# Optimization experiments

Hardware: AMD Instinct MI355X
Metric: run time of the kernel (lower is better)

The kernel has to match this reference:

```python
import jax, jax.numpy as jnp
import numpy as np
import math

L_MAX = 4
NUM_LM = (L_MAX + 1) ** 2  # 25
DEG_OF_LM = np.repeat(np.arange(L_MAX + 1), 2 * np.arange(L_MAX + 1) + 1)
SL = [slice(l * l, (l + 1) * (l + 1)) for l in range(L_MAX + 1)]
CUTOFF = 5.0

def _lf(n):
    return math.lgamma(n + 1)

def _cg_complex(l1, m1, l2, m2, l3, m3):
    if m1 + m2 != m3 or l3 < abs(l1 - l2) or l3 > l1 + l2:
        return 0.0
    pre = 0.5 * (_lf(l1 + l2 - l3) + _lf(l1 - l2 + l3) + _lf(-l1 + l2 + l3)
                 - _lf(l1 + l2 + l3 + 1)
                 + _lf(l1 + m1) + _lf(l1 - m1) + _lf(l2 + m2) + _lf(l2 - m2)
                 + _lf(l3 + m3) + _lf(l3 - m3))
    kmin = max(0, l2 - l3 - m1, l1 - l3 + m2)
    kmax = min(l1 + l2 - l3, l1 - m1, l2 + m2)
    s = 0.0
    for k in range(kmin, kmax + 1):
        ln = (_lf(k) + _lf(l1 + l2 - l3 - k) + _lf(l1 - m1 - k) + _lf(l2 + m2 - k)
              + _lf(l3 - l2 + m1 + k) + _lf(l3 - l1 - m2 + k))
        s += (-1) ** k * math.exp(pre - ln)
    return math.sqrt(2 * l3 + 1) * s

def _build_real_cg():
    # complex CG (Racah) -> real-spherical-harmonic coupling coefficients
    Cc = np.zeros((NUM_LM, NUM_LM, NUM_LM), dtype=np.complex128)
    U = np.zeros((NUM_LM, NUM_LM), dtype=np.complex128)
    for l in range(L_MAX + 1):
        off = l * l + l
        U[off, off] = 1.0
        for m in range(1, l + 1):
            U[off + m, off + m] = (-1) ** m / np.sqrt(2)
            U[off + m, off - m] = 1 / np.sqrt(2)
            U[off - m, off - m] = 1j / np.sqrt(2)
            U[off - m, off + m] = -1j * (-1) ** m / np.sqrt(2)
    for l1 in range(L_MAX + 1):
        for l2 in range(L_MAX + 1):
            for l3 in range(abs(l1 - l2), min(L_MAX, l1 + l2) + 1):
                for m1 in range(-l1, l1 + 1):
                    for m2 in range(-l2, l2 + 1):
                        m3 = m1 + m2
                        if abs(m3) <= l3:
                            Cc[l1*l1+l1+m1, l2*l2+l2+m2, l3*l3+l3+m3] = _cg_complex(l1, m1, l2, m2, l3, m3)
    T = np.einsum('ia,jb,kc,abc->ijk', U, U, U.conj(), Cc)
    C = T.real + T.imag  # exactly one part is nonzero per entry
    C[np.abs(C) < 1e-12] = 0.0
    return C.astype(np.float32)

CG = jnp.asarray(_build_real_cg())
PATHS = [(l1, l2, l3) for l1 in range(L_MAX + 1) for l2 in range(L_MAX + 1)
         for l3 in range(abs(l1 - l2), min(L_MAX, l1 + l2) + 1)]

def real_sph_harm(u):
    x, y, z = u[..., 0], u[..., 1], u[..., 2]
    x2, y2, z2 = x*x, y*y, z*z
    pi = np.pi
    Y = [
        jnp.full_like(x, 0.5*np.sqrt(1/pi)),
        np.sqrt(3/(4*pi))*y, np.sqrt(3/(4*pi))*z, np.sqrt(3/(4*pi))*x,
        0.5*np.sqrt(15/pi)*x*y, 0.5*np.sqrt(15/pi)*y*z,
        0.25*np.sqrt(5/pi)*(3*z2-1), 0.5*np.sqrt(15/pi)*x*z,
        0.25*np.sqrt(15/pi)*(x2-y2),
        0.25*np.sqrt(35/(2*pi))*y*(3*x2-y2), 0.5*np.sqrt(105/pi)*x*y*z,
        0.25*np.sqrt(21/(2*pi))*y*(5*z2-1), 0.25*np.sqrt(7/pi)*z*(5*z2-3),
        0.25*np.sqrt(21/(2*pi))*x*(5*z2-1), 0.25*np.sqrt(105/pi)*z*(x2-y2),
        0.25*np.sqrt(35/(2*pi))*x*(x2-3*y2),
        0.75*np.sqrt(35/pi)*x*y*(x2-y2), 0.75*np.sqrt(35/(2*pi))*y*z*(3*x2-y2),
        0.75*np.sqrt(5/pi)*x*y*(7*z2-1), 0.75*np.sqrt(5/(2*pi))*y*z*(7*z2-3),
        (3/16)*np.sqrt(1/pi)*(35*z2*z2-30*z2+3),
        0.75*np.sqrt(5/(2*pi))*x*z*(7*z2-3),
        (3/8)*np.sqrt(5/pi)*(x2-y2)*(7*z2-1),
        0.75*np.sqrt(35/(2*pi))*x*z*(x2-3*y2),
        (3/16)*np.sqrt(35/pi)*(x2*x2-6*x2*y2+y2*y2),
    ]
    return jnp.stack(Y, axis=-1)  # [..., 25]

def degree_dense(x, W):
    # equivariant per-(parity, degree) dense: x [N,2,25,Fi], W [2,5,Fi,Fo]
    return jnp.einsum('nplf,plfg->nplg', x, W[:, DEG_OF_LM])

def tensor_product(a, b, w):
    # CG tensor product with per-(path, parity-pair, feature) weights w [P,2,2,F]
    N, _, _, F = a.shape
    out = jnp.zeros((N, 2, NUM_LM, F), a.dtype)
    for pi, (l1, l2, l3) in enumerate(PATHS):
        cg = CG[SL[l1], SL[l2], SL[l3]]
        tmp = jnp.einsum('npaf,nqbf,abc->npqcf', a[:, :, SL[l1]], b[:, :, SL[l2]], cg)
        s = (l1 + l2 + l3) % 2  # output parity channel for (p1,p2) even combos
        wp = w[pi]
        even = wp[0, 0] * tmp[:, 0, 0] + wp[1, 1] * tmp[:, 1, 1]
        odd = wp[0, 1] * tmp[:, 0, 1] + wp[1, 0] * tmp[:, 1, 0]
        out = out.at[:, s, SL[l3]].add(even)
        out = out.at[:, 1 - s, SL[l3]].add(odd)
    return out

def _forward(atomic_numbers, neighbour_indices, neighbour_displacements,
             Wsp, emb_table, W_et, b_et, norm,
             td0_W1, td0_W2, td0_wp, td1_W1, td1_W2, td1_wp, w_fused):
    N = atomic_numbers.shape[0]
    idx_i = neighbour_indices[:, 0]
    idx_j = neighbour_indices[:, 1]
    Z_j = atomic_numbers[idx_j]
    # species-aware radial basis x real spherical harmonics
    r = jnp.sqrt(jnp.sum(neighbour_displacements**2, axis=-1) + 1e-12)
    u = neighbour_displacements / r[:, None]
    K = Wsp.shape[1]
    centers = jnp.linspace(0.0, CUTOFF, K)
    gamma = (K / CUTOFF) ** 2
    fcut = 0.5 * (jnp.cos(np.pi * jnp.clip(r / CUTOFF, 0.0, 1.0)) + 1.0)
    rbf = jnp.exp(-gamma * (r[:, None] - centers) ** 2) * fcut[:, None]
    g = jnp.einsum('ek,ekr->er', rbf, Wsp[Z_j])  # gather-by-Z_j mixing [E,R]
    Ye = real_sph_harm(u)  # [E,25]
    edge_feats = Ye[:, :, None] * g[:, None, :]  # [E,25,R]
    # irregular scatter-sum over neighbours -> per-atom features
    y0 = jax.ops.segment_sum(edge_feats, idx_i, num_segments=N) / norm
    y = jnp.stack([y0, jnp.zeros_like(y0)], axis=1)  # [N,2,25,R], pseudotensors zero
    ylist = [y]
    for W1, W2, wp in ((td0_W1, td0_W2, td0_wp), (td1_W1, td1_W2, td1_wp)):
        a = degree_dense(ylist[-1], W1)
        b = degree_dense(ylist[-1], W2)
        ylist.append(tensor_product(a, b, wp))  # TensorDense moment layer
    y = jnp.concatenate(ylist, axis=-1)  # [N,2,25,Fe]
    te = emb_table[atomic_numbers] @ W_et + b_et  # transformed embedding [N,Fe]
    # fused tensor: scalar embedding x multi-degree features (paths (0,l,l))
    y = te[:, None, None, :] * y * w_fused[:, DEG_OF_LM][None]
    y = y.at[:, 0, 0, :].add(te)  # scalar residual connection
    return y + y * jnp.tanh(jax.nn.softplus(y))  # y + mish(y)

def setup_inputs() -> dict:
    key = jax.random.key(0)
    ks = jax.random.split(key, 13)
    N, E = 10000, 160000
    S, D, R, F = 95, 64, 16, 64
    Fe = R + 2 * F
    sn = lambda k, shape, fan: jax.random.normal(k, shape, jnp.float32) / np.sqrt(fan)
    return {
        'atomic_numbers': jax.random.randint(ks[0], (N,), 0, S),
        'neighbour_indices': jax.random.randint(ks[1], (E, 2), 0, N),
        'neighbour_displacements': jax.random.normal(ks[2], (E, 3), jnp.float32) * 1.5,
        'Wsp': sn(ks[3], (S, R, R), R),
        'emb_table': sn(ks[4], (S, D), 1),
        'W_et': sn(ks[5], (D, Fe), D),
        'b_et': jnp.zeros((Fe,), jnp.float32),
        'norm': jnp.full((1,), E / N, jnp.float32),
        'td0_W1': sn(ks[6], (2, 5, R, F), R),
        'td0_W2': sn(ks[7], (2, 5, R, F), R),
        'td0_wp': sn(ks[8], (len(PATHS), 2, 2, F), 4),
        'td1_W1': sn(ks[9], (2, 5, F, F), F),
        'td1_W2': sn(ks[10], (2, 5, F, F), F),
        'td1_wp': sn(ks[11], (len(PATHS), 2, 2, F), 4),
        'w_fused': sn(ks[12], (2, 5, Fe), 1),
    }

def reference(atomic_numbers, neighbour_indices, neighbour_displacements,
              Wsp, emb_table, W_et, b_et, norm,
              td0_W1, td0_W2, td0_wp, td1_W1, td1_W2, td1_wp, w_fused):
    return _forward(atomic_numbers, neighbour_indices, neighbour_displacements,
                    Wsp, emb_table, W_et, b_et, norm,
                    td0_W1, td0_W2, td0_wp, td1_W1, td1_W2, td1_wp, w_fused)
```

## Files before the change

kernel.cpp:

```cpp
#include <hip/hip_runtime.h>
#include <math.h>


constexpr double FTAB[14]={1.0,1.0,2.0,6.0,24.0,120.0,720.0,5040.0,40320.0,362880.0,
                           3628800.0,39916800.0,479001600.0,6227020800.0};

constexpr double csqrt_(double x){
  if(x<=0.0) return 0.0;
  double g = x<1.0 ? 1.0 : x;
  for(int i=0;i<60;i++){
    double ng=0.5*(g+x/g);
    if(ng==g) break;
    g=ng;
  }
  return g;
}

constexpr double cgc_(int l1,int m1,int l2,int m2,int l3,int m3){
  if(m1+m2!=m3) return 0.0;
  int ad = l1>l2 ? l1-l2 : l2-l1;
  if(l3<ad || l3>l1+l2) return 0.0;
  double P=FTAB[l1+l2-l3]*FTAB[l1-l2+l3]*FTAB[-l1+l2+l3]/FTAB[l1+l2+l3+1]
          *FTAB[l1+m1]*FTAB[l1-m1]*FTAB[l2+m2]*FTAB[l2-m2]*FTAB[l3+m3]*FTAB[l3-m3];
  double spre=csqrt_(P);
  int kmin=0; if(l2-l3-m1>kmin)kmin=l2-l3-m1; if(l1-l3+m2>kmin)kmin=l1-l3+m2;
  int kmax=l1+l2-l3; if(l1-m1<kmax)kmax=l1-m1; if(l2+m2<kmax)kmax=l2+m2;
  double s=0.0;
  for(int k=kmin;k<=kmax;k++){
    double den=FTAB[k]*FTAB[l1+l2-l3-k]*FTAB[l1-m1-k]*FTAB[l2+m2-k]
              *FTAB[l3-l2+m1+k]*FTAB[l3-l1-m2+k];
    s+=((k&1)?-1.0:1.0)/den;
  }
  return csqrt_((double)(2*l3+1))*spre*s;
}

constexpr int lof_(int idx){ int l=0; while((l+1)*(l+1)<=idx) l++; return l; }

struct U2 { int c[2]; double re[2], im[2]; int n; };
constexpr U2 urow_(int idx){
  int l=lof_(idx);
  const double is2=0.70710678118654752440;
  U2 u{}; int off=l*l+l, m=idx-off;
  if(m==0){ u.c[0]=off; u.re[0]=1.0; u.im[0]=0.0; u.n=1; return u; }
  if(m>0){
    double sgn=(m&1)?-1.0:1.0;
    u.c[0]=off+m; u.re[0]=sgn*is2; u.im[0]=0.0;
    u.c[1]=off-m; u.re[1]=is2;     u.im[1]=0.0;
    u.n=2; return u;
  }
  int mm=-m; double sgn=(mm&1)?-1.0:1.0;
  u.c[0]=off-mm; u.re[0]=0.0; u.im[0]=is2;
  u.c[1]=off+mm; u.re[1]=0.0; u.im[1]=-sgn*is2;
  u.n=2; return u;
}

constexpr double realCG_(int i,int j,int k){
  int li=lof_(i), lj=lof_(j), lk=lof_(k);
  U2 ua=urow_(i), ub=urow_(j), uc=urow_(k);
  double Tre=0.0,Tim=0.0;
  for(int a=0;a<ua.n;a++)for(int b=0;b<ub.n;b++)for(int c=0;c<uc.n;c++){
    int ma=ua.c[a]-li*li-li, mb=ub.c[b]-lj*lj-lj, mc=uc.c[c]-lk*lk-lk;
    double cg=cgc_(li,ma,lj,mb,lk,mc);
    if(cg==0.0) continue;
    double xre=ua.re[a]*ub.re[b]-ua.im[a]*ub.im[b];
    double xim=ua.re[a]*ub.im[b]+ua.im[a]*ub.re[b];
    double wre=xre*uc.re[c]+xim*uc.im[c];
    double wim=xim*uc.re[c]-xre*uc.im[c];
    Tre+=wre*cg; Tim+=wim*cg;
  }
  double C=Tre+Tim;
  if(C<1e-12 && C>-1e-12) C=0.0;
  return C;
}

constexpr int path_l(int pi,int which){
  int idx=0;
  for(int l1=0;l1<=4;l1++)for(int l2=0;l2<=4;l2++){
    int lo = l1>l2 ? l1-l2 : l2-l1;
    int hi = (l1+l2<4)?(l1+l2):4;
    for(int l3=lo;l3<=hi;l3++){
      if(idx==pi) return which==0?l1:(which==1?l2:l3);
      idx++;
    }
  }
  return 0;
}

struct EntryList { int n; signed char ia[81]; signed char ib[81]; float v[81]; };

template<int L1,int L2,int L3,int C>
constexpr EntryList build_slot(){
  EntryList E{};
  for(int a=0;a<2*L1+1;a++)for(int b=0;b<2*L2+1;b++){
    double val=realCG_(L1*L1+a, L2*L2+b, L3*L3+C);
    if(val!=0.0){ E.ia[E.n]=(signed char)a; E.ib[E.n]=(signed char)b; E.v[E.n]=(float)val; E.n++; }
  }
  return E;
}
template<int L1,int L2,int L3,int C>
struct SlotTab { static constexpr EntryList E = build_slot<L1,L2,L3,C>(); };

template<int...I> struct iseq{};
template<int N,int...I> struct mkseq : mkseq<N-1,N-1,I...>{};
template<int...I> struct mkseq<0,I...>{ using type=iseq<I...>; };

__device__ __forceinline__ float rl(float v,int k){
  return __int_as_float(__builtin_amdgcn_readlane(__float_as_int(v),k));
}


template<int L3,int PI,int C>
__device__ __forceinline__ void t0_slot(const float(&a)[25],const float(&b)[25],
                                        float(&o0)[9],float(&o1)[9],float w00){
  constexpr int L1=path_l(PI,0),L2=path_l(PI,1);
  using ST=SlotTab<L1,L2,L3,C>;
  if constexpr(ST::E.n>0){
    float r=0.f;
    #pragma unroll
    for(int j=0;j<ST::E.n;j++)
      r += ST::E.v[j]*a[L1*L1+(int)ST::E.ia[j]]*b[L2*L2+(int)ST::E.ib[j]];
    constexpr int Sp=(L1+L2+L3)&1;
    if constexpr(Sp==0) o0[C]+=w00*r; else o1[C]+=w00*r;
  }
}
template<int L3,int PI,int...Cs>
__device__ __forceinline__ void t0_cs(iseq<Cs...>,const float(&a)[25],const float(&b)[25],
                                      float(&o0)[9],float(&o1)[9],float w00){
  (t0_slot<L3,PI,Cs>(a,b,o0,o1,w00), ...);
}
template<int L3,int PI>
__device__ __forceinline__ void t0_path(const float(&a)[25],const float(&b)[25],
                                        float(&o0)[9],float(&o1)[9],const float* __restrict__ wp,int f){
  if constexpr(path_l(PI,2)==L3){
    float w00=wp[PI*256+f];
    t0_cs<L3,PI>(typename mkseq<2*L3+1>::type{}, a,b,o0,o1,w00);
  }
}
template<int L3,int...PIs>
__device__ __forceinline__ void t0_l3(iseq<PIs...>,const float(&a)[25],const float(&b)[25],
                                      const float* __restrict__ wp,int f,float* __restrict__ yo){
  float o0[9],o1[9];
  #pragma unroll
  for(int c=0;c<9;c++){o0[c]=0.f;o1[c]=0.f;}
  (t0_path<L3,PIs>(a,b,o0,o1,wp,f), ...);
  #pragma unroll
  for(int c=0;c<2*L3+1;c++){
    yo[(L3*L3+c)*144+f]      = o0[c];
    yo[3600+(L3*L3+c)*144+f] = o1[c];
  }
}


template<int L3,int PI,int C>
__device__ __forceinline__ void t1_slot(const float(&a0)[25],const float(&a1)[25],
                                        const float(&b0)[25],const float(&b1)[25],
                                        float(&o0)[9],float(&o1)[9],
                                        float w00,float w01,float w10,float w11){
  constexpr int L1=path_l(PI,0),L2=path_l(PI,1);
  using ST=SlotTab<L1,L2,L3,C>;
  if constexpr(ST::E.n>0){
    float r00=0.f,r01=0.f,r10=0.f,r11=0.f;
    #pragma unroll
    for(int j=0;j<ST::E.n;j++){
      constexpr_helper: ;
      float v=ST::E.v[j];
      float av0=a0[L1*L1+(int)ST::E.ia[j]], av1=a1[L1*L1+(int)ST::E.ia[j]];
      float bv0=b0[L2*L2+(int)ST::E.ib[j]], bv1=b1[L2*L2+(int)ST::E.ib[j]];
      float p=v*av0, q=v*av1;
      r00+=p*bv0; r01+=p*bv1; r10+=q*bv0; r11+=q*bv1;
    }
    constexpr int Sp=(L1+L2+L3)&1;
    float ev=w00*r00+w11*r11, od=w01*r01+w10*r10;
    if constexpr(Sp==0){ o0[C]+=ev; o1[C]+=od; }
    else               { o1[C]+=ev; o0[C]+=od; }
  }
}
template<int L3,int PI,int...Cs>
__device__ __forceinline__ void t1_cs(iseq<Cs...>,const float(&a0)[25],const float(&a1)[25],
                                      const float(&b0)[25],const float(&b1)[25],
                                      float(&o0)[9],float(&o1)[9],
                                      float w00,float w01,float w10,float w11){
  (t1_slot<L3,PI,Cs>(a0,a1,b0,b1,o0,o1,w00,w01,w10,w11), ...);
}
template<int L3,int PI>
__device__ __forceinline__ void t1_path(const float(&a0)[25],const float(&a1)[25],
                                        const float(&b0)[25],const float(&b1)[25],
                                        float(&o0)[9],float(&o1)[9],const float* __restrict__ wp,int f){
  if constexpr(path_l(PI,2)==L3){
    const float* wpp=wp+PI*256+f;
    float w00=wpp[0], w01=wpp[64], w10=wpp[128], w11=wpp[192];
    t1_cs<L3,PI>(typename mkseq<2*L3+1>::type{}, a0,a1,b0,b1,o0,o1,w00,w01,w10,w11);
  }
}
template<int L3,int...PIs>
__device__ __forceinline__ void t1_l3(iseq<PIs...>,const float(&a0)[25],const float(&a1)[25],
                                      const float(&b0)[25],const float(&b1)[25],
                                      const float* __restrict__ wp,int f,float* __restrict__ yo){
  float o0[9],o1[9];
  #pragma unroll
  for(int c=0;c<9;c++){o0[c]=0.f;o1[c]=0.f;}
  (t1_path<L3,PIs>(a0,a1,b0,b1,o0,o1,wp,f), ...);
  #pragma unroll
  for(int c=0;c<2*L3+1;c++){
    yo[(L3*L3+c)*144+f]      = o0[c];
    yo[3600+(L3*L3+c)*144+f] = o1[c];
  }
}


__global__ __launch_bounds__(256) void k_zero(int* cnt, int N){
  int t=blockIdx.x*256+threadIdx.x; if(t<N) cnt[t]=0;
}


__global__ __launch_bounds__(256) void k_edge(const int* __restrict__ Z, const int* __restrict__ nbr,
    const float* __restrict__ disp, const float* __restrict__ Wsp,
    float* __restrict__ g, float* __restrict__ Ye, int* cnt, int E){
  int e=blockIdx.x*256+threadIdx.x; if(e>=E) return;
  int i0=nbr[2*e], j0=nbr[2*e+1];
  atomicAdd(&cnt[i0],1);
  int z=Z[j0];
  float dx=disp[3*e], dy=disp[3*e+1], dz=disp[3*e+2];
  float r=sqrtf(dx*dx+dy*dy+dz*dz+1e-12f);
  float inv=1.0f/r;
  float x=dx*inv, y=dy*inv, zz=dz*inv;
  float rc=fminf(r*0.2f,1.0f);
  float fc=0.5f*(cosf(3.14159265358979323846f*rc)+1.0f);
  float rbf[16];
  #pragma unroll
  for(int k=0;k<16;k++){
    float d=r-(float)k*(5.0f/15.0f);
    rbf[k]=expf(-10.24f*d*d)*fc;
  }
  const float* Wz=Wsp + z*256;
  #pragma unroll
  for(int rr=0;rr<16;rr++){
    float s=0.f;
    #pragma unroll
    for(int k=0;k<16;k++) s += rbf[k]*Wz[k*16+rr];
    g[e*16+rr]=s;
  }
  float x2=x*x,y2=y*y,z2=zz*zz;
  float* Y=Ye+(size_t)e*25;
  Y[0]=0.28209479177387814f;
  Y[1]=0.4886025119029199f*y;
  Y[2]=0.4886025119029199f*zz;
  Y[3]=0.4886025119029199f*x;
  Y[4]=1.0925484305920792f*x*y;
  Y[5]=1.0925484305920792f*y*zz;
  Y[6]=0.31539156525252005f*(3.f*z2-1.f);
  Y[7]=1.0925484305920792f*x*zz;
  Y[8]=0.5462742152960396f*(x2-y2);
  Y[9]=0.5900435899266435f*y*(3.f*x2-y2);
  Y[10]=2.890611442640554f*x*y*zz;
  Y[11]=0.4570457994644658f*y*(5.f*z2-1.f);
  Y[12]=0.3731763325901154f*zz*(5.f*z2-3.f);
  Y[13]=0.4570457994644658f*x*(5.f*z2-1.f);
  Y[14]=1.445305721320277f*zz*(x2-y2);
  Y[15]=0.5900435899266435f*x*(x2-3.f*y2);
  Y[16]=2.5033429417967046f*x*y*(x2-y2);
  Y[17]=1.7701307697799304f*y*zz*(3.f*x2-y2);
  Y[18]=0.9461746957575601f*x*y*(7.f*z2-1.f);
  Y[19]=0.6690465435572892f*y*zz*(7.f*z2-3.f);
  Y[20]=0.10578554691520431f*(35.f*z2*z2-30.f*z2+3.f);
  Y[21]=0.6690465435572892f*x*zz*(7.f*z2-3.f);
  Y[22]=0.47308734787878004f*(x2-y2)*(7.f*z2-1.f);
  Y[23]=1.7701307697799304f*x*zz*(x2-3.f*y2);
  Y[24]=0.6258357354491761f*(x2*x2-6.f*x2*y2+y2*y2);
}


__global__ __launch_bounds__(1024) void k_scan(const int* __restrict__ cnt, int* offs, int* cursor, int N){
  __shared__ int part[1024];
  int t=threadIdx.x;
  int per=(N+1023)>>10;
  int start=t*per;
  int s=0;
  for(int i2=0;i2<per;i2++){int idx=start+i2; if(idx<N) s+=cnt[idx];}
  part[t]=s; __syncthreads();
  for(int off=1;off<1024;off<<=1){
    int v=(t>=off)?part[t-off]:0;
    __syncthreads();
    part[t]+=v;
    __syncthreads();
  }
  int run=(t>0)?part[t-1]:0;
  for(int i2=0;i2<per;i2++){int idx=start+i2; if(idx<N){offs[idx]=run; cursor[idx]=run; run+=cnt[idx];}}
  if(t==1023) offs[N]=part[1023];
}

__global__ __launch_bounds__(256) void k_fill(const int* __restrict__ nbr, int* cursor, int* elist, int E){
  int e=blockIdx.x*256+threadIdx.x; if(e>=E)return;
  int pos=atomicAdd(&cursor[nbr[2*e]],1);
  elist[pos]=e;
}


__global__ __launch_bounds__(64) void k_agg(const float* __restrict__ g, const float* __restrict__ Ye,
    const int* __restrict__ offs, const int* __restrict__ elist, const float* __restrict__ norm,
    float* __restrict__ y){
  int n=blockIdx.x, t=threadIdx.x;
  __shared__ float gs[16];
  __shared__ float ys[25];
  float acc[7];
  #pragma unroll
  for(int i2=0;i2<7;i2++) acc[i2]=0.f;
  int e0=offs[n], e1=offs[n+1];
  for(int ei=e0; ei<e1; ei++){
    int e=elist[ei];
    if(t<16) gs[t]=g[(size_t)e*16+t];
    else if(t<41) ys[t-16]=Ye[(size_t)e*25+t-16];
    __syncthreads();
    #pragma unroll
    for(int i2=0;i2<7;i2++){
      int o=t+64*i2;
      if(o<400) acc[i2] += ys[o>>4]*gs[o&15];
    }
    __syncthreads();
  }
  float nv=1.0f/norm[0];
  float* yo=y+(size_t)n*7200;
  #pragma unroll
  for(int i2=0;i2<7;i2++){
    int o=t+64*i2;
    if(o<400){ int lm=o>>4,k=o&15; yo[lm*144+k]=acc[i2]*nv; yo[3600+lm*144+k]=0.f; }
  }
}


__global__ __launch_bounds__(64,4) void k_tp0(float* __restrict__ y, const float* __restrict__ W1,
    const float* __restrict__ W2, const float* __restrict__ wp){
  int n=blockIdx.x, f=threadIdx.x;
  float* ybase = y + (size_t)n*7200;
  float a[25],b[25];
  #pragma unroll
  for(int i=0;i<25;i++){a[i]=0.f;b[i]=0.f;}
  #pragma unroll
  for(int l=0;l<5;l++){
    const int n1=2*l+1, base=l*l;
    float yk[9];
    #pragma unroll
    for(int j=0;j<n1;j++) yk[j]=ybase[(base+j)*144+f];
    const float* w1=W1+l*1024+f;
    const float* w2=W2+l*1024+f;
    #pragma unroll 8
    for(int k=0;k<16;k++){
      float u1=w1[k*64], u2=w2[k*64];
      #pragma unroll
      for(int j=0;j<n1;j++){
        float yv=rl(yk[j],k);
        a[base+j]+=yv*u1; b[base+j]+=yv*u2;
      }
    }
  }
  float* yo=ybase+16;
  t0_l3<0>(typename mkseq<65>::type{}, a,b,wp,f,yo);
  t0_l3<1>(typename mkseq<65>::type{}, a,b,wp,f,yo);
  t0_l3<2>(typename mkseq<65>::type{}, a,b,wp,f,yo);
  t0_l3<3>(typename mkseq<65>::type{}, a,b,wp,f,yo);
  t0_l3<4>(typename mkseq<65>::type{}, a,b,wp,f,yo);
}


__global__ __launch_bounds__(64,3) void k_tp1(float* __restrict__ y, const float* __restrict__ W1,
    const float* __restrict__ W2, const float* __restrict__ wp){
  int n=blockIdx.x, f=threadIdx.x;
  float* ybase = y + (size_t)n*7200;
  const float* yin = ybase + 16;
  float a0[25],a1[25],b0[25],b1[25];
  #pragma unroll
  for(int i=0;i<25;i++){a0[i]=0.f;a1[i]=0.f;b0[i]=0.f;b1[i]=0.f;}
  #pragma unroll
  for(int p=0;p<2;p++){
    #pragma unroll
    for(int l=0;l<5;l++){
      const int n1=2*l+1, base=l*l;
      float yk[9];
      #pragma unroll
      for(int j=0;j<n1;j++) yk[j]=yin[p*3600+(base+j)*144+f];
      const float* w1=W1+(p*5+l)*4096+f;
      const float* w2=W2+(p*5+l)*4096+f;
      #pragma unroll 8
      for(int k=0;k<64;k++){
        float u1=w1[k*64], u2=w2[k*64];
        #pragma unroll
        for(int j=0;j<n1;j++){
          float yv=rl(yk[j],k);
          if(p==0){ a0[base+j]+=yv*u1; b0[base+j]+=yv*u2; }
          else    { a1[base+j]+=yv*u1; b1[base+j]+=yv*u2; }
        }
      }
    }
  }
  float* yo=ybase+80;
  t1_l3<0>(typename mkseq<65>::type{}, a0,a1,b0,b1,wp,f,yo);
  t1_l3<1>(typename mkseq<65>::type{}, a0,a1,b0,b1,wp,f,yo);
  t1_l3<2>(typename mkseq<65>::type{}, a0,a1,b0,b1,wp,f,yo);
  t1_l3<3>(typename mkseq<65>::type{}, a0,a1,b0,b1,wp,f,yo);
  t1_l3<4>(typename mkseq<65>::type{}, a0,a1,b0,b1,wp,f,yo);
}


__device__ const int DEGLM[25]={0,1,1,1,2,2,2,2,2,3,3,3,3,3,3,3,4,4,4,4,4,4,4,4,4};

__global__ __launch_bounds__(128) void k_final(float* __restrict__ y, const int* __restrict__ Z,
    const float* __restrict__ emb, const float* __restrict__ Wet, const float* __restrict__ bet,
    const float* __restrict__ wf){
  int n=blockIdx.x, t=threadIdx.x;
  __shared__ float embs[64];
  __shared__ float teS[144];
  int z=Z[n];
  if(t<64) embs[t]=emb[z*64+t];
  __syncthreads();
  for(int c=t;c<144;c+=128){
    float s=bet[c];
    for(int d=0;d<64;d++) s+=embs[d]*Wet[d*144+c];
    teS[c]=s;
  }
  __syncthreads();
  float* yo=y+(size_t)n*7200;
  for(int row=0;row<50;row++){
    int p=row/25, lm=row-25*p;
    const float* wrow=wf+(p*5+DEGLM[lm])*144;
    for(int c=t;c<144;c+=128){
      float v=yo[row*144+c];
      float te=teS[c];
      v=te*v*wrow[c];
      if(row==0) v+=te;
      float sp=log1pf(expf(v));
      v=v+v*tanhf(sp);
      yo[row*144+c]=v;
    }
  }
}


extern "C" void kernel_launch(void* const* d_in, const int* in_sizes, int n_in,
                              void* d_out, int out_size, void* d_ws, size_t ws_size,
                              hipStream_t stream) {
  const int*   Z    =(const int*)  d_in[0];
  const int*   nbr  =(const int*)  d_in[1];
  const float* disp =(const float*)d_in[2];
  const float* Wsp  =(const float*)d_in[3];
  const float* emb  =(const float*)d_in[4];
  const float* Wet  =(const float*)d_in[5];
  const float* bet  =(const float*)d_in[6];
  const float* norm =(const float*)d_in[7];
  const float* t0W1 =(const float*)d_in[8];
  const float* t0W2 =(const float*)d_in[9];
  const float* t0wp =(const float*)d_in[10];
  const float* t1W1 =(const float*)d_in[11];
  const float* t1W2 =(const float*)d_in[12];
  const float* t1wp =(const float*)d_in[13];
  const float* wf   =(const float*)d_in[14];
  int N=in_sizes[0];
  int E=in_sizes[1]/2;
  float* y=(float*)d_out;

  char* w=(char*)d_ws;
  size_t off=0;
  auto take=[&](size_t bytes)->void*{ size_t cur=(off+255)&~(size_t)255; off=cur+bytes; return (void*)(w+cur); };
  int*   cnt   =(int*)  take((size_t)N*4);
  int*   offs  =(int*)  take((size_t)(N+1)*4);
  int*   cursor=(int*)  take((size_t)N*4);
  int*   elist =(int*)  take((size_t)E*4);
  float* g     =(float*)take((size_t)E*16*4);
  float* Ye    =(float*)take((size_t)E*25*4);
  (void)ws_size; (void)out_size; (void)n_in;

  k_zero   <<<dim3((N+255)/256),   dim3(256), 0, stream>>>(cnt, N);
  k_edge   <<<dim3((E+255)/256),   dim3(256), 0, stream>>>(Z, nbr, disp, Wsp, g, Ye, cnt, E);
  k_scan   <<<dim3(1),             dim3(1024),0, stream>>>(cnt, offs, cursor, N);
  k_fill   <<<dim3((E+255)/256),   dim3(256), 0, stream>>>(nbr, cursor, elist, E);
  k_agg    <<<dim3(N),             dim3(64),  0, stream>>>(g, Ye, offs, elist, norm, y);
  k_tp0    <<<dim3(N),             dim3(64),  0, stream>>>(y, t0W1, t0W2, t0wp);
  k_tp1    <<<dim3(N),             dim3(64),  0, stream>>>(y, t1W1, t1W2, t1wp);
  k_final  <<<dim3(N),             dim3(128), 0, stream>>>(y, Z, emb, Wet, bet, wf);
}
```

Before: 1.584 ms.

## Fuse both tensor-product layers and final activation into one per-node kernel

Result: slower. 6.200 ms (+291.4%).

```diff
diff --git a/kernel.cpp b/kernel.cpp
--- a/kernel.cpp
+++ b/kernel.cpp
@@ -108,6 +108,11 @@
   return __int_as_float(__builtin_amdgcn_readlane(__float_as_int(v),k));
 }
 
+__device__ __forceinline__ float actv(float v){
+  float sp=log1pf(expf(v));
+  return v+v*tanhf(sp);
+}
+
 
 template<int L3,int PI,int C>
 __device__ __forceinline__ void t0_slot(const float(&a)[25],const float(&b)[25],
@@ -137,16 +142,16 @@
   }
 }
 template<int L3,int...PIs>
-__device__ __forceinline__ void t0_l3(iseq<PIs...>,const float(&a)[25],const float(&b)[25],
-                                      const float* __restrict__ wp,int f,float* __restrict__ yo){
+__device__ __forceinline__ void t0_l3r(iseq<PIs...>,const float(&a)[25],const float(&b)[25],
+                                       const float* __restrict__ wp,int f,float(&t0out)[50]){
   float o0[9],o1[9];
   #pragma unroll
   for(int c=0;c<9;c++){o0[c]=0.f;o1[c]=0.f;}
   (t0_path<L3,PIs>(a,b,o0,o1,wp,f), ...);
   #pragma unroll
   for(int c=0;c<2*L3+1;c++){
-    yo[(L3*L3+c)*144+f]      = o0[c];
-    yo[3600+(L3*L3+c)*144+f] = o1[c];
+    t0out[L3*L3+c]    = o0[c];
+    t0out[25+L3*L3+c] = o1[c];
   }
 }
 
@@ -162,7 +167,6 @@
     float r00=0.f,r01=0.f,r10=0.f,r11=0.f;
     #pragma unroll
     for(int j=0;j<ST::E.n;j++){
-      constexpr_helper: ;
       float v=ST::E.v[j];
       float av0=a0[L1*L1+(int)ST::E.ia[j]], av1=a1[L1*L1+(int)ST::E.ia[j]];
       float bv0=b0[L2*L2+(int)ST::E.ib[j]], bv1=b1[L2*L2+(int)ST::E.ib[j]];
@@ -193,17 +197,27 @@
   }
 }
 template<int L3,int...PIs>
-__device__ __forceinline__ void t1_l3(iseq<PIs...>,const float(&a0)[25],const float(&a1)[25],
-                                      const float(&b0)[25],const float(&b1)[25],
-                                      const float* __restrict__ wp,int f,float* __restrict__ yo){
+__device__ __forceinline__ void t1_l3w(iseq<PIs...>,const float(&a0)[25],const float(&a1)[25],
+                                       const float(&b0)[25],const float(&b1)[25],
+                                       const float* __restrict__ wp,int f,
+                                       float* __restrict__ ybase,
+                                       const float* __restrict__ wf,float te2){
   float o0[9],o1[9];
   #pragma unroll
   for(int c=0;c<9;c++){o0[c]=0.f;o1[c]=0.f;}
   (t1_path<L3,PIs>(a0,a1,b0,b1,o0,o1,wp,f), ...);
+  float w0v=wf[L3*144+80+f];
+  float w1v=wf[(5+L3)*144+80+f];
   #pragma unroll
   for(int c=0;c<2*L3+1;c++){
-    yo[(L3*L3+c)*144+f]      = o0[c];
-    yo[3600+(L3*L3+c)*144+f] = o1[c];
+    int lm=L3*L3+c;
+    float v0=te2*o0[c]*w0v;
+    if(L3==0&&c==0) v0+=te2;
+    v0=actv(v0);
+    ybase[lm*144+80+f]=v0;
+    float v1=te2*o1[c]*w1v;
+    v1=actv(v1);
+    ybase[(25+lm)*144+80+f]=v1;
   }
 }
 
@@ -323,114 +337,128 @@
   #pragma unroll
   for(int i2=0;i2<7;i2++){
     int o=t+64*i2;
-    if(o<400){ int lm=o>>4,k=o&15; yo[lm*144+k]=acc[i2]*nv; yo[3600+lm*144+k]=0.f; }
-  }
-}
-
-
-__global__ __launch_bounds__(64,4) void k_tp0(float* __restrict__ y, const float* __restrict__ W1,
-    const float* __restrict__ W2, const float* __restrict__ wp){
-  int n=blockIdx.x, f=threadIdx.x;
-  float* ybase = y + (size_t)n*7200;
-  float a[25],b[25];
-  #pragma unroll
-  for(int i=0;i<25;i++){a[i]=0.f;b[i]=0.f;}
-  #pragma unroll
-  for(int l=0;l<5;l++){
-    const int n1=2*l+1, base=l*l;
-    float yk[9];
-    #pragma unroll
-    for(int j=0;j<n1;j++) yk[j]=ybase[(base+j)*144+f];
-    const float* w1=W1+l*1024+f;
-    const float* w2=W2+l*1024+f;
-    #pragma unroll 8
-    for(int k=0;k<16;k++){
-      float u1=w1[k*64], u2=w2[k*64];
-      #pragma unroll
-      for(int j=0;j<n1;j++){
-        float yv=rl(yk[j],k);
-        a[base+j]+=yv*u1; b[base+j]+=yv*u2;
-      }
-    }
-  }
-  float* yo=ybase+16;
-  t0_l3<0>(typename mkseq<65>::type{}, a,b,wp,f,yo);
-  t0_l3<1>(typename mkseq<65>::type{}, a,b,wp,f,yo);
-  t0_l3<2>(typename mkseq<65>::type{}, a,b,wp,f,yo);
-  t0_l3<3>(typename mkseq<65>::type{}, a,b,wp,f,yo);
-  t0_l3<4>(typename mkseq<65>::type{}, a,b,wp,f,yo);
-}
-
-
-__global__ __launch_bounds__(64,3) void k_tp1(float* __restrict__ y, const float* __restrict__ W1,
-    const float* __restrict__ W2, const float* __restrict__ wp){
-  int n=blockIdx.x, f=threadIdx.x;
-  float* ybase = y + (size_t)n*7200;
-  const float* yin = ybase + 16;
-  float a0[25],a1[25],b0[25],b1[25];
-  #pragma unroll
-  for(int i=0;i<25;i++){a0[i]=0.f;a1[i]=0.f;b0[i]=0.f;b1[i]=0.f;}
-  #pragma unroll
-  for(int p=0;p<2;p++){
-    #pragma unroll
-    for(int l=0;l<5;l++){
-      const int n1=2*l+1, base=l*l;
-      float yk[9];
-      #pragma unroll
-      for(int j=0;j<n1;j++) yk[j]=yin[p*3600+(base+j)*144+f];
-      const float* w1=W1+(p*5+l)*4096+f;
-      const float* w2=W2+(p*5+l)*4096+f;
-      #pragma unroll 8
-      for(int k=0;k<64;k++){
-        float u1=w1[k*64], u2=w2[k*64];
-        #pragma unroll
-        for(int j=0;j<n1;j++){
-          float yv=rl(yk[j],k);
-          if(p==0){ a0[base+j]+=yv*u1; b0[base+j]+=yv*u2; }
-          else    { a1[base+j]+=yv*u1; b1[base+j]+=yv*u2; }
-        }
-      }
-    }
-  }
-  float* yo=ybase+80;
-  t1_l3<0>(typename mkseq<65>::type{}, a0,a1,b0,b1,wp,f,yo);
-  t1_l3<1>(typename mkseq<65>::type{}, a0,a1,b0,b1,wp,f,yo);
-  t1_l3<2>(typename mkseq<65>::type{}, a0,a1,b0,b1,wp,f,yo);
-  t1_l3<3>(typename mkseq<65>::type{}, a0,a1,b0,b1,wp,f,yo);
-  t1_l3<4>(typename mkseq<65>::type{}, a0,a1,b0,b1,wp,f,yo);
-}
-
-
-__device__ const int DEGLM[25]={0,1,1,1,2,2,2,2,2,3,3,3,3,3,3,3,4,4,4,4,4,4,4,4,4};
-
-__global__ __launch_bounds__(128) void k_final(float* __restrict__ y, const int* __restrict__ Z,
-    const float* __restrict__ emb, const float* __restrict__ Wet, const float* __restrict__ bet,
-    const float* __restrict__ wf){
+    if(o<400){ int lm=o>>4,k=o&15; yo[lm*144+k]=acc[i2]*nv; }
+  }
+}
+
+
+__global__ __launch_bounds__(128) void k_te(const int* __restrict__ Z, const float* __restrict__ emb,
+    const float* __restrict__ Wet, const float* __restrict__ bet, float* __restrict__ te){
   int n=blockIdx.x, t=threadIdx.x;
   __shared__ float embs[64];
-  __shared__ float teS[144];
   int z=Z[n];
   if(t<64) embs[t]=emb[z*64+t];
   __syncthreads();
   for(int c=t;c<144;c+=128){
     float s=bet[c];
     for(int d=0;d<64;d++) s+=embs[d]*Wet[d*144+c];
-    teS[c]=s;
-  }
-  __syncthreads();
-  float* yo=y+(size_t)n*7200;
-  for(int row=0;row<50;row++){
-    int p=row/25, lm=row-25*p;
-    const float* wrow=wf+(p*5+DEGLM[lm])*144;
-    for(int c=t;c<144;c+=128){
-      float v=yo[row*144+c];
-      float te=teS[c];
-      v=te*v*wrow[c];
-      if(row==0) v+=te;
-      float sp=log1pf(expf(v));
-      v=v+v*tanhf(sp);
-      yo[row*144+c]=v;
-    }
+    te[(size_t)n*144+c]=s;
+  }
+}
+
+
+__global__ __launch_bounds__(64) __attribute__((amdgpu_waves_per_eu(1,2)))
+void k_tp(float* __restrict__ y,
+          const float* __restrict__ W1_0, const float* __restrict__ W2_0, const float* __restrict__ wp0,
+          const float* __restrict__ W1_1, const float* __restrict__ W2_1, const float* __restrict__ wp1,
+          const float* __restrict__ te, const float* __restrict__ wf){
+  int n=blockIdx.x, f=threadIdx.x;
+  float* ybase = y + (size_t)n*7200;
+
+  float y0r[25];
+  #pragma unroll
+  for(int lm=0;lm<25;lm++) y0r[lm]=ybase[lm*144+(f&15)];
+
+  float a[25],b[25];
+  #pragma unroll
+  for(int i=0;i<25;i++){a[i]=0.f;b[i]=0.f;}
+  #pragma unroll
+  for(int l=0;l<5;l++){
+    const int n1=2*l+1, base=l*l;
+    const float* w1=W1_0+l*1024+f;
+    const float* w2=W2_0+l*1024+f;
+    #pragma unroll 8
+    for(int k=0;k<16;k++){
+      float u1=w1[k*64], u2=w2[k*64];
+      #pragma unroll
+      for(int j=0;j<n1;j++){
+        float yv=rl(y0r[base+j],k);
+        a[base+j]+=yv*u1; b[base+j]+=yv*u2;
+      }
+    }
+  }
+
+  {
+    float te0=te[(size_t)n*144+(f&15)];
+    #pragma unroll
+    for(int lm=0;lm<25;lm++){
+      float wv=wf[lof_(lm)*144+(f&15)];
+      float v=te0*y0r[lm]*wv;
+      if(lm==0) v+=te0;
+      v=actv(v);
+      if(f<16){
+        ybase[lm*144+f]=v;
+        ybase[(25+lm)*144+f]=0.f;
+      }
+    }
+  }
+
+  float t0out[50];
+  t0_l3r<0>(typename mkseq<65>::type{}, a,b,wp0,f,t0out);
+  t0_l3r<1>(typename mkseq<65>::type{}, a,b,wp0,f,t0out);
+  t0_l3r<2>(typename mkseq<65>::type{}, a,b,wp0,f,t0out);
+  t0_l3r<3>(typename mkseq<65>::type{}, a,b,wp0,f,t0out);
+  t0_l3r<4>(typename mkseq<65>::type{}, a,b,wp0,f,t0out);
+
+  float a0[25],a1[25],b0[25],b1[25];
+  #pragma unroll
+  for(int i=0;i<25;i++){a0[i]=0.f;a1[i]=0.f;b0[i]=0.f;b1[i]=0.f;}
+  #pragma unroll
+  for(int p=0;p<2;p++){
+    #pragma unroll
+    for(int l=0;l<5;l++){
+      const int n1=2*l+1, base=l*l;
+      const float* w1=W1_1+(p*5+l)*4096+f;
+      const float* w2=W2_1+(p*5+l)*4096+f;
+      #pragma unroll 8
+      for(int k=0;k<64;k++){
+        float u1=w1[k*64], u2=w2[k*64];
+        #pragma unroll
+        for(int j=0;j<n1;j++){
+          float yv=rl(t0out[p*25+base+j],k);
+          if(p==0){ a0[base+j]+=yv*u1; b0[base+j]+=yv*u2; }
+          else    { a1[base+j]+=yv*u1; b1[base+j]+=yv*u2; }
+        }
+      }
+    }
+  }
+
+  {
+    float te1=te[(size_t)n*144+16+f];
+    #pragma unroll
+    for(int p=0;p<2;p++){
+      #pragma unroll
+      for(int l=0;l<5;l++){
+        float wv=wf[(p*5+l)*144+16+f];
+        #pragma unroll
+        for(int j=0;j<2*l+1;j++){
+          int row=p*25+l*l+j;
+          float v=te1*t0out[row]*wv;
+          if(p==0&&l==0&&j==0) v+=te1;
+          v=actv(v);
+          ybase[row*144+16+f]=v;
+        }
+      }
+    }
+  }
+
+  {
+    float te2=te[(size_t)n*144+80+f];
+    t1_l3w<0>(typename mkseq<65>::type{}, a0,a1,b0,b1,wp1,f,ybase,wf,te2);
+    t1_l3w<1>(typename mkseq<65>::type{}, a0,a1,b0,b1,wp1,f,ybase,wf,te2);
+    t1_l3w<2>(typename mkseq<65>::type{}, a0,a1,b0,b1,wp1,f,ybase,wf,te2);
+    t1_l3w<3>(typename mkseq<65>::type{}, a0,a1,b0,b1,wp1,f,ybase,wf,te2);
+    t1_l3w<4>(typename mkseq<65>::type{}, a0,a1,b0,b1,wp1,f,ybase,wf,te2);
   }
 }
 
@@ -466,6 +494,7 @@
   int*   elist =(int*)  take((size_t)E*4);
   float* g     =(float*)take((size_t)E*16*4);
   float* Ye    =(float*)take((size_t)E*25*4);
+  float* te    =(float*)take((size_t)N*144*4);
   (void)ws_size; (void)out_size; (void)n_in;
 
   k_zero   <<<dim3((N+255)/256),   dim3(256), 0, stream>>>(cnt, N);
@@ -473,7 +502,6 @@
   k_scan   <<<dim3(1),             dim3(1024),0, stream>>>(cnt, offs, cursor, N);
   k_fill   <<<dim3((E+255)/256),   dim3(256), 0, stream>>>(nbr, cursor, elist, E);
   k_agg    <<<dim3(N),             dim3(64),  0, stream>>>(g, Ye, offs, elist, norm, y);
-  k_tp0    <<<dim3(N),             dim3(64),  0, stream>>>(y, t0W1, t0W2, t0wp);
-  k_tp1    <<<dim3(N),             dim3(64),  0, stream>>>(y, t1W1, t1W2, t1wp);
-  k_final  <<<dim3(N),             dim3(128), 0, stream>>>(y, Z, emb, Wet, bet, wf);
-}
+  k_te     <<<dim3(N),             dim3(128), 0, stream>>>(Z, emb, Wet, bet, te);
+  k_tp     <<<dim3(N),             dim3(64),  0, stream>>>(y, t0W1, t0W2, t0wp, t1W1, t1W2, t1wp, te, wf);
+}
```
